# Kernel tuning notes

Hardware: AMD Instinct MI355X
Metric: run time of the kernel (lower is better)

Reference implementation:

```python
import jax, jax.numpy as jnp
import numpy as np

B, L, D, H, NL, F, C = 32, 512, 512, 8, 6, 2048, 9
HD = D // H
SCALE = float(np.sqrt(HD))
EPS = 1e-5


def _layernorm(x, g, b):
    mu = jnp.mean(x, axis=-1, keepdims=True)
    var = jnp.mean((x - mu) ** 2, axis=-1, keepdims=True)
    return (x - mu) * jax.lax.rsqrt(var + EPS) * g + b


def setup_inputs() -> dict:
    key = jax.random.key(0)
    ks = jax.random.split(key, 16)
    s = 0.02
    return {
        "x": jax.random.normal(ks[0], (B, L, D), jnp.float32),
        "case_ids": jax.random.randint(ks[1], (B, L), 0, C),
        "attention_mask": jnp.ones((B, L), jnp.int32),
        "Wq": jax.random.normal(ks[2], (NL, D, D), jnp.float32) * s,
        "bq": jnp.zeros((NL, D), jnp.float32),
        "Wk": jax.random.normal(ks[3], (NL, D, D), jnp.float32) * s,
        "bk": jnp.zeros((NL, D), jnp.float32),
        "Wv": jax.random.normal(ks[4], (NL, D, D), jnp.float32) * s,
        "bv": jnp.zeros((NL, D), jnp.float32),
        "Wo": jax.random.normal(ks[5], (NL, D, D), jnp.float32) * s,
        "bo": jnp.zeros((NL, D), jnp.float32),
        "ln1_g": jnp.ones((NL, D), jnp.float32),
        "ln1_b": jnp.zeros((NL, D), jnp.float32),
        "ln2_g": jnp.ones((NL, D), jnp.float32),
        "ln2_b": jnp.zeros((NL, D), jnp.float32),
        "W1": jax.random.normal(ks[6], (NL, D, F), jnp.float32) * s,
        "b1": jnp.zeros((NL, F), jnp.float32),
        "W2": jax.random.normal(ks[7], (NL, F, D), jnp.float32) * s,
        "b2": jnp.zeros((NL, D), jnp.float32),
        "case_bias": jax.random.normal(ks[8], (NL, H, C, C), jnp.float32) * 0.1,
        "verb_bias": jax.random.normal(ks[9], (NL, H), jnp.float32) * 0.1,
        "fn_g": jnp.ones((D,), jnp.float32),
        "fn_b": jnp.zeros((D,), jnp.float32),
    }


def reference(x, case_ids, attention_mask, Wq, bq, Wk, bk, Wv, bv, Wo, bo,
              ln1_g, ln1_b, ln2_g, ln2_b, W1, b1, W2, b2,
              case_bias, verb_bias, fn_g, fn_b):
    dt = x.dtype
    # causal + padding additive mask: [B, 1, L, L]
    causal = jnp.triu(jnp.full((L, L), -10000.0, dtype=dt), k=1)[None, None]
    pad = (1.0 - attention_mask.astype(dt))[:, None, None, :] * -10000.0
    mask = causal + pad
    verb_mask = (case_ids == 8).astype(dt)  # [B, L]
    ci, cj = case_ids[:, :, None], case_ids[:, None, :]  # [B,L,1], [B,1,L]

    for i in range(NL):
        h = _layernorm(x, ln1_g[i], ln1_b[i])
        q = (h @ Wq[i] + bq[i]).reshape(B, L, H, HD).transpose(0, 2, 1, 3)
        k = (h @ Wk[i] + bk[i]).reshape(B, L, H, HD).transpose(0, 2, 1, 3)
        v = (h @ Wv[i] + bv[i]).reshape(B, L, H, HD).transpose(0, 2, 1, 3)
        scores = jnp.einsum('bhqd,bhkd->bhqk', q, k) / SCALE
        # Panini grammatical bias: per-head pairwise case bias + verb key bias
        pbias = case_bias[i][:, ci, cj]  # [H, B, L, L]
        scores = scores + jnp.transpose(pbias, (1, 0, 2, 3))
        scores = scores + verb_bias[i][None, :, None, None] * verb_mask[:, None, None, :]
        scores = scores + mask
        w = jax.nn.softmax(scores, axis=-1)
        attn = jnp.einsum('bhqk,bhkd->bhqd', w, v).transpose(0, 2, 1, 3).reshape(B, L, D)
        x = x + attn @ Wo[i] + bo[i]
        h2 = _layernorm(x, ln2_g[i], ln2_b[i])
        ff = jax.nn.gelu(h2 @ W1[i] + b1[i], approximate=False) @ W2[i] + b2[i]
        x = x + ff
    return _layernorm(x, fn_g, fn_b)
```

## Files before the change

### kernel.cpp

```cpp
#include <hip/hip_runtime.h>
#include <hip/hip_bf16.h>

#define B_   32
#define L_   512
#define D_   512
#define H_   8
#define NL_  6
#define F_   2048
#define C_   9
#define HD_  64
#define MTOK 16384

typedef __bf16 bf16x8 __attribute__((ext_vector_type(8)));
typedef __bf16 bf16x4 __attribute__((ext_vector_type(4)));
typedef float  f32x4  __attribute__((ext_vector_type(4)));

#define MFMA16(a,b,c) __builtin_amdgcn_mfma_f32_16x16x32_bf16((a),(b),(c),0,0,0)
#define GLD16(g,l) __builtin_amdgcn_global_load_lds( \
    (const __attribute__((address_space(1))) void*)(g), \
    (__attribute__((address_space(3))) void*)(l), 16, 0, 0)

__global__ __launch_bounds__(256) void transpose_w(
    const float* __restrict__ in, __hip_bfloat16* __restrict__ out,
    int K, int N, size_t zso)
{
    __shared__ float t[32][33];
    const int z = blockIdx.z;
    const float* src = in + (size_t)z * K * N;
    __hip_bfloat16* dst = out + (size_t)z * zso;
    const int n0 = blockIdx.x * 32, k0 = blockIdx.y * 32;
    const int tx = threadIdx.x, ty = threadIdx.y;
#pragma unroll
    for (int r = ty; r < 32; r += 8)
        t[r][tx] = src[(size_t)(k0 + r) * N + n0 + tx];
    __syncthreads();
#pragma unroll
    for (int r = ty; r < 32; r += 8)
        dst[(size_t)(n0 + r) * K + k0 + tx] = __float2bfloat16(t[tx][r]);
}

__global__ void copy_f32x4(const float4* __restrict__ in, float4* __restrict__ out, int n)
{
    int i = blockIdx.x * blockDim.x + threadIdx.x;
    if (i < n) out[i] = in[i];
}

template <typename OUT>
__global__ __launch_bounds__(256) void ln_kernel(
    const float* __restrict__ x, const float* __restrict__ g,
    const float* __restrict__ be, OUT* __restrict__ out)
{
    const int row  = blockIdx.x * 4 + (threadIdx.x >> 6);
    const int lane = threadIdx.x & 63;
    const int c0   = lane * 8;
    const float* xr = x + (size_t)row * D_ + c0;
    float4 a = *(const float4*)xr;
    float4 c = *(const float4*)(xr + 4);
    float v[8] = {a.x, a.y, a.z, a.w, c.x, c.y, c.z, c.w};

    float s = 0.f;
#pragma unroll
    for (int j = 0; j < 8; ++j) s += v[j];
#pragma unroll
    for (int o = 1; o < 64; o <<= 1) s += __shfl_xor(s, o, 64);
    const float mu = s * (1.0f / D_);

    float s2 = 0.f;
#pragma unroll
    for (int j = 0; j < 8; ++j) { float d = v[j] - mu; s2 += d * d; }
#pragma unroll
    for (int o = 1; o < 64; o <<= 1) s2 += __shfl_xor(s2, o, 64);
    const float rs = rsqrtf(s2 * (1.0f / D_) + 1e-5f);

    float4 g0 = *(const float4*)(g + c0);
    float4 g1 = *(const float4*)(g + c0 + 4);
    float4 b0 = *(const float4*)(be + c0);
    float4 b1 = *(const float4*)(be + c0 + 4);
    float gg[8] = {g0.x, g0.y, g0.z, g0.w, g1.x, g1.y, g1.z, g1.w};
    float bb[8] = {b0.x, b0.y, b0.z, b0.w, b1.x, b1.y, b1.z, b1.w};

    if constexpr (sizeof(OUT) == 2) {
        bf16x8 o8;
#pragma unroll
        for (int j = 0; j < 8; ++j)
            o8[j] = (__bf16)((v[j] - mu) * rs * gg[j] + bb[j]);
        *(bf16x8*)((__hip_bfloat16*)out + (size_t)row * D_ + c0) = o8;
    } else {
        float* op = (float*)out + (size_t)row * D_ + c0;
        float4 r0, r1;
        r0.x = (v[0]-mu)*rs*gg[0]+bb[0]; r0.y = (v[1]-mu)*rs*gg[1]+bb[1];
        r0.z = (v[2]-mu)*rs*gg[2]+bb[2]; r0.w = (v[3]-mu)*rs*gg[3]+bb[3];
        r1.x = (v[4]-mu)*rs*gg[4]+bb[4]; r1.y = (v[5]-mu)*rs*gg[5]+bb[5];
        r1.z = (v[6]-mu)*rs*gg[6]+bb[6]; r1.w = (v[7]-mu)*rs*gg[7]+bb[7];
        *(float4*)op = r0; *(float4*)(op + 4) = r1;
    }
}

template <int EPI, int WNW>
__global__ __launch_bounds__(512, 2) void gemm_p(
    const __hip_bfloat16* __restrict__ A,
    const __hip_bfloat16* __restrict__ BT,
    const float* __restrict__ bias0, const float* __restrict__ bias1,
    const float* __restrict__ bias2,
    void* __restrict__ out0, void* __restrict__ out1, void* __restrict__ out2,
    const float* __restrict__ Res, int Ndim, int K)
{
    constexpr int FM = (WNW == 4) ? 8 : 4;
    constexpr int BN = WNW * 64;
    constexpr int BLOADS = BN / 128;
    __shared__ __align__(16) __hip_bfloat16 As[4][256 * 32];
    __shared__ __align__(16) __hip_bfloat16 Bs[4][BN * 32];

    const int tid = threadIdx.x;
    const int w = tid >> 6, lane = tid & 63;
    const int lq = lane & 15, lg = lane >> 4;

    const int gX = gridDim.x;
    const int nwg = gX * gridDim.y;
    int flat = blockIdx.y * gX + blockIdx.x;
    {
        const int qq = nwg >> 3, rr = nwg & 7;
        const int xcd = flat & 7, off = flat >> 3;
        flat = (xcd < rr ? xcd * (qq + 1) : rr * (qq + 1) + (xcd - rr) * qq) + off;
    }
    const int bx = flat % gX, by = flat / gX;
    const int m0 = by * 256, n0 = bx * BN;
    const int wm = w / WNW, wn = w % WNW;
    const int RB = wm * (FM * 16);
    const int CB = wn * 64;

    const int sr = lane >> 2;
    const int sc = ((lane & 3) ^ ((lane >> 3) & 3)) * 8;
    const __hip_bfloat16* gA0 = A + (size_t)(m0 + (w*2+0)*16 + sr) * K + sc;
    const __hip_bfloat16* gA1 = A + (size_t)(m0 + (w*2+1)*16 + sr) * K + sc;
    const __hip_bfloat16* gB0;
    const __hip_bfloat16* gB1 = nullptr;
    if constexpr (BLOADS == 2) {
        gB0 = BT + (size_t)(n0 + (w*2+0)*16 + sr) * K + sc;
        gB1 = BT + (size_t)(n0 + (w*2+1)*16 + sr) * K + sc;
    } else {
        gB0 = BT + (size_t)(n0 + w*16 + sr) * K + sc;
    }

    auto STAGE = [&](int tt) {
        const size_t ko = (size_t)tt * 32;
        char* ab = (char*)As[tt & 3];
        GLD16(gA0 + ko, ab + (w*2+0) * 1024);
        GLD16(gA1 + ko, ab + (w*2+1) * 1024);
        char* bb = (char*)Bs[tt & 3];
        if constexpr (BLOADS == 2) {
            GLD16(gB0 + ko, bb + (w*2+0) * 1024);
            GLD16(gB1 + ko, bb + (w*2+1) * 1024);
        } else {
            GLD16(gB0 + ko, bb + w * 1024);
        }
    };

    const int rsw = (lq >> 1) & 3;
    const int aoff = (RB + lq) * 64 + ((lg ^ rsw) << 4);
    const int boff = (CB + lq) * 64 + ((lg ^ rsw) << 4);

    f32x4 acc[FM][4] = {};
    const int NTt = K >> 5;

    STAGE(0); STAGE(1); STAGE(2);

    for (int t = 0; t < NTt; ++t) {
        if (t < NTt - 2) {
            if constexpr (BLOADS == 2) asm volatile("s_waitcnt vmcnt(8)" ::: "memory");
            else                       asm volatile("s_waitcnt vmcnt(6)" ::: "memory");
        } else if (t < NTt - 1) {
            if constexpr (BLOADS == 2) asm volatile("s_waitcnt vmcnt(4)" ::: "memory");
            else                       asm volatile("s_waitcnt vmcnt(3)" ::: "memory");
        } else {
            asm volatile("s_waitcnt vmcnt(0)" ::: "memory");
        }
        __builtin_amdgcn_s_barrier();
        __builtin_amdgcn_sched_barrier(0);

        const char* ca = (const char*)As[t & 3];
        const char* cb = (const char*)Bs[t & 3];
        bf16x8 bf[4];
#pragma unroll
        for (int fn = 0; fn < 4; ++fn) bf[fn] = *(const bf16x8*)(cb + boff + fn * 1024);
        bf16x8 af[FM];
#pragma unroll
        for (int fm = 0; fm < FM; ++fm) af[fm] = *(const bf16x8*)(ca + aoff + fm * 1024);

        if (t + 3 < NTt) STAGE(t + 3);

        __builtin_amdgcn_s_setprio(1);
#pragma unroll
        for (int fm = 0; fm < FM; ++fm)
#pragma unroll
            for (int fn = 0; fn < 4; ++fn)
                acc[fm][fn] = MFMA16(af[fm], bf[fn], acc[fm][fn]);
        __builtin_amdgcn_s_setprio(0);
    }

    if constexpr (EPI == 4) {
        const int sec = n0 >> 9;
        const int nb = (n0 & 511) + CB;
        const float* bp = sec == 0 ? bias0 : (sec == 1 ? bias1 : bias2);
        float bcol[4];
#pragma unroll
        for (int fn = 0; fn < 4; ++fn) bcol[fn] = bp[nb + fn * 16 + lq];
        if (sec < 2) {
            __hip_bfloat16* op = (__hip_bfloat16*)(sec == 0 ? out0 : out1);
#pragma unroll
            for (int fm = 0; fm < FM; ++fm)
#pragma unroll
                for (int fn = 0; fn < 4; ++fn)
#pragma unroll
                    for (int r = 0; r < 4; ++r) {
                        const int m = m0 + RB + fm * 16 + lg * 4 + r;
                        op[(size_t)m * 512 + nb + fn * 16 + lq] =
                            __float2bfloat16(acc[fm][fn][r] + bcol[fn]);
                    }
        } else {
            __hip_bfloat16* vp = (__hip_bfloat16*)out2;
            const int bb = m0 >> 9;
            const int l0 = (m0 & 511) + RB + lg * 4;
#pragma unroll
            for (int fm = 0; fm < FM; ++fm)
#pragma unroll
                for (int fn = 0; fn < 4; ++fn) {
                    bf16x4 pv;
#pragma unroll
                    for (int r = 0; r < 4; ++r)
                        pv[r] = (__bf16)(acc[fm][fn][r] + bcol[fn]);
                    *(bf16x4*)(vp + ((size_t)(bb * 512 + nb + fn * 16 + lq)) * 512
                               + l0 + fm * 16) = pv;
                }
        }
    } else {
        float bcol[4];
#pragma unroll
        for (int fn = 0; fn < 4; ++fn) bcol[fn] = bias0[n0 + CB + fn * 16 + lq];
#pragma unroll
        for (int fm = 0; fm < FM; ++fm)
#pragma unroll
            for (int fn = 0; fn < 4; ++fn) {
                const int n = n0 + CB + fn * 16 + lq;
#pragma unroll
                for (int r = 0; r < 4; ++r) {
                    const int m = m0 + RB + fm * 16 + lg * 4 + r;
                    float v = acc[fm][fn][r] + bcol[fn];
                    if constexpr (EPI == 1) {
                        float* Co = (float*)out0;
                        const size_t idx = (size_t)m * Ndim + n;
                        Co[idx] = Res[idx] + v;
                    } else {
                        float gl = 0.5f * v * (1.0f + erff(v * 0.70710678118654752f));
                        ((__hip_bfloat16*)out0)[(size_t)m * Ndim + n] = __float2bfloat16(gl);
                    }
                }
            }
    }
}

__global__ __launch_bounds__(256) void attn_kernel(
    const __hip_bfloat16* __restrict__ Q, const __hip_bfloat16* __restrict__ K,
    const __hip_bfloat16* __restrict__ VT, __hip_bfloat16* __restrict__ Out,
    const int* __restrict__ case_ids, const int* __restrict__ amask,
    const float* __restrict__ case_bias, const float* __restrict__ verb_bias,
    int layer)
{
    __shared__ __align__(16) __bf16 Ks[2][64 * 64];
    __shared__ __align__(16) __bf16 Vs[2][64 * 64];
    __shared__ __align__(16) __bf16 Pl[4][16 * 64];
    __shared__ __bf16 Bia[9][520];

    const int bh = blockIdx.x;
    const int b = bh >> 3, hh = bh & 7;
    const int qc = blockIdx.y;
    const int t = threadIdx.x;
    const int w = t >> 6, lane = t & 63;
    const int lq = lane & 15, lg = lane >> 4;
    const int swz = lq & 7;

    const int rA = w * 16 + (lane >> 3);
    const int swsrc = ((lane & 7) ^ (lane >> 3)) << 4;
    const __hip_bfloat16* kg0 = K  + ((size_t)b * L_ + rA) * D_ + hh * HD_;
    const __hip_bfloat16* vg0 = VT + ((size_t)b * D_ + hh * HD_ + rA) * L_;

    auto stage = [&](int buf, int kv0) {
        const char* gk = (const char*)(kg0 + (size_t)kv0 * D_) + swsrc;
        GLD16(gk,                      (char*)Ks[buf] + w * 2048);
        GLD16(gk + (size_t)8 * D_ * 2, (char*)Ks[buf] + w * 2048 + 1024);
        const char* gv = (const char*)(vg0 + kv0) + swsrc;
        GLD16(gv,                      (char*)Vs[buf] + w * 2048);
        GLD16(gv + (size_t)8 * L_ * 2, (char*)Vs[buf] + w * 2048 + 1024);
    };

    stage(0, 0);

    const float vb = verb_bias[layer * H_ + hh];
    const float* cb = case_bias + ((size_t)layer * H_ + hh) * (C_ * C_);
    for (int idx = t; idx < 9 * 512; idx += 256) {
        const int ci = idx >> 9, kv = idx & 511;
        const int cj = case_ids[b * L_ + kv];
        Bia[ci][kv] = (__bf16)(cb[ci * C_ + cj] + (cj == 8 ? vb : 0.f)
                               - 10000.f * (1.f - (float)amask[b * L_ + kv]));
    }
    __syncthreads();

    const int qloc = w * 16 + lq;
    const int qrow = qc * 64 + qloc;
    const int ci_q = case_ids[b * L_ + qrow];
    const __hip_bfloat16* qp = Q + ((size_t)b * L_ + qrow) * D_ + hh * HD_;
    const bf16x8 qf0 = *(const bf16x8*)(qp + lg * 8);
    const bf16x8 qf1 = *(const bf16x8*)(qp + 32 + lg * 8);

    float m_run = -1e30f, l_run = 0.f;
    f32x4 o[4] = {};
    const int ntiles = qc + 1;
    int cur = 0;

    for (int kt = 0; kt < ntiles; ++kt) {
        if (kt + 1 < ntiles) stage(cur ^ 1, (kt + 1) * 64);

        const char* kb  = (const char*)Ks[cur];
        const char* vb2 = (const char*)Vs[cur];

        f32x4 s[4] = {};
        __builtin_amdgcn_s_setprio(1);
#pragma unroll
        for (int c = 0; c < 4; ++c) {
            const bf16x8 ka = *(const bf16x8*)(kb + (16 * c + lq) * 128 + ((lg ^ swz) << 4));
            s[c] = MFMA16(ka, qf0, s[c]);
            const bf16x8 kc = *(const bf16x8*)(kb + (16 * c + lq) * 128 + (((4 + lg) ^ swz) << 4));
            s[c] = MFMA16(kc, qf1, s[c]);
        }
        __builtin_amdgcn_s_setprio(0);

        const __bf16* brow = &Bia[ci_q][kt * 64];
        const bool dtile = (kt == qc);
        float xs[16];
#pragma unroll
        for (int c = 0; c < 4; ++c) {
            const bf16x4 bb = *(const bf16x4*)(brow + 16 * c + lg * 4);
#pragma unroll
            for (int r = 0; r < 4; ++r) {
                const int kvl = 16 * c + lg * 4 + r;
                float v = s[c][r] * 0.125f + (float)bb[r];
                xs[4 * c + r] = (dtile && (kvl > qloc)) ? -1e9f : v;
            }
        }

        float a0 = fmaxf(fmaxf(xs[0], xs[1]),  fmaxf(xs[2], xs[3]));
        float a1 = fmaxf(fmaxf(xs[4], xs[5]),  fmaxf(xs[6], xs[7]));
        float a2 = fmaxf(fmaxf(xs[8], xs[9]),  fmaxf(xs[10], xs[11]));
        float a3 = fmaxf(fmaxf(xs[12], xs[13]), fmaxf(xs[14], xs[15]));
        float pmax = fmaxf(fmaxf(a0, a1), fmaxf(a2, a3));
        pmax = fmaxf(pmax, __shfl_xor(pmax, 16, 64));
        pmax = fmaxf(pmax, __shfl_xor(pmax, 32, 64));

        const float mnew = fmaxf(m_run, pmax);
        const float corr = __expf(m_run - mnew);
        float p[16], ps0 = 0.f, ps1 = 0.f;
#pragma unroll
        for (int j = 0; j < 16; j += 2) {
            p[j]     = __expf(xs[j] - mnew);     ps0 += p[j];
            p[j + 1] = __expf(xs[j + 1] - mnew); ps1 += p[j + 1];
        }
        float ps = ps0 + ps1;
        ps += __shfl_xor(ps, 16, 64);
        ps += __shfl_xor(ps, 32, 64);
        l_run = l_run * corr + ps;
        m_run = mnew;

        float cr[4];
#pragma unroll
        for (int r = 0; r < 4; ++r) cr[r] = __shfl(corr, lg * 4 + r, 64);
#pragma unroll
        for (int nt = 0; nt < 4; ++nt)
#pragma unroll
            for (int r = 0; r < 4; ++r) o[nt][r] *= cr[r];

        char* pw = (char*)Pl[w];
#pragma unroll
        for (int c = 0; c < 4; ++c) {
            bf16x4 pv;
#pragma unroll
            for (int r = 0; r < 4; ++r) pv[r] = (__bf16)p[4 * c + r];
            const int slot = (2 * c + (lg >> 1)) ^ swz;
            *(bf16x4*)(pw + lq * 128 + (slot << 4) + ((lg & 1) << 3)) = pv;
        }

        __builtin_amdgcn_s_setprio(1);
#pragma unroll
        for (int hf = 0; hf < 2; ++hf) {
            const bf16x8 pf = *(const bf16x8*)(pw + lq * 128 + (((hf * 4 + lg) ^ swz) << 4));
#pragma unroll
            for (int nt = 0; nt < 4; ++nt) {
                const bf16x8 vf = *(const bf16x8*)(vb2 + (nt * 16 + lq) * 128
                                                   + (((hf * 4 + lg) ^ swz) << 4));
                o[nt] = MFMA16(pf, vf, o[nt]);
            }
        }
        __builtin_amdgcn_s_setprio(0);

        __syncthreads();
        cur ^= 1;
    }

    const float inv = 1.f / l_run;
    float ir[4];
#pragma unroll
    for (int r = 0; r < 4; ++r) ir[r] = __shfl(inv, lg * 4 + r, 64);
    __hip_bfloat16* op = Out + ((size_t)b * L_ + qc * 64 + w * 16) * D_ + hh * HD_;
#pragma unroll
    for (int nt = 0; nt < 4; ++nt)
#pragma unroll
        for (int r = 0; r < 4; ++r)
            op[(size_t)(lg * 4 + r) * D_ + nt * 16 + lq] = __float2bfloat16(o[nt][r] * ir[r]);
}

extern "C" void kernel_launch(void* const* d_in, const int* in_sizes, int n_in,
                              void* d_out, int out_size, void* d_ws, size_t ws_size,
                              hipStream_t stream)
{
    const float* x_in  = (const float*)d_in[0];
    const int*   cids  = (const int*)  d_in[1];
    const int*   amask = (const int*)  d_in[2];
    const float* Wq = (const float*)d_in[3];
    const float* bq = (const float*)d_in[4];
    const float* Wk = (const float*)d_in[5];
    const float* bk = (const float*)d_in[6];
    const float* Wv = (const float*)d_in[7];
    const float* bv = (const float*)d_in[8];
    const float* Wo = (const float*)d_in[9];
    const float* bo = (const float*)d_in[10];
    const float* ln1g = (const float*)d_in[11];
    const float* ln1b = (const float*)d_in[12];
    const float* ln2g = (const float*)d_in[13];
    const float* ln2b = (const float*)d_in[14];
    const float* W1 = (const float*)d_in[15];
    const float* b1 = (const float*)d_in[16];
    const float* W2 = (const float*)d_in[17];
    const float* b2 = (const float*)d_in[18];
    const float* cbias = (const float*)d_in[19];
    const float* vbias = (const float*)d_in[20];
    const float* fng = (const float*)d_in[21];
    const float* fnb = (const float*)d_in[22];

    char* w = (char*)d_ws;
    float* x_ws = (float*)w;                 w += (size_t)MTOK * D_ * 4;
    __hip_bfloat16* hbuf = (__hip_bfloat16*)w; w += (size_t)MTOK * D_ * 2;
    __hip_bfloat16* qbuf = (__hip_bfloat16*)w; w += (size_t)MTOK * D_ * 2;
    __hip_bfloat16* kbuf = (__hip_bfloat16*)w; w += (size_t)MTOK * D_ * 2;
    __hip_bfloat16* vtb  = (__hip_bfloat16*)w; w += (size_t)MTOK * D_ * 2;
    __hip_bfloat16* ffb  = (__hip_bfloat16*)w; w += (size_t)MTOK * F_ * 2;
    __hip_bfloat16* WqkvT = (__hip_bfloat16*)w; w += (size_t)NL_ * 3 * D_ * D_ * 2;
    __hip_bfloat16* WoT  = (__hip_bfloat16*)w; w += (size_t)NL_ * D_ * D_ * 2;
    __hip_bfloat16* W1T  = (__hip_bfloat16*)w; w += (size_t)NL_ * D_ * F_ * 2;
    __hip_bfloat16* W2T  = (__hip_bfloat16*)w; w += (size_t)NL_ * D_ * F_ * 2;

    const size_t qkvZ = (size_t)3 * D_ * D_;
    const dim3 tb(32, 8);
    transpose_w<<<dim3(D_/32, D_/32, NL_), tb, 0, stream>>>(Wq, WqkvT,           D_, D_, qkvZ);
    transpose_w<<<dim3(D_/32, D_/32, NL_), tb, 0, stream>>>(Wk, WqkvT + D_*D_,   D_, D_, qkvZ);
    transpose_w<<<dim3(D_/32, D_/32, NL_), tb, 0, stream>>>(Wv, WqkvT + 2*D_*D_, D_, D_, qkvZ);
    transpose_w<<<dim3(D_/32, D_/32, NL_), tb, 0, stream>>>(Wo, WoT, D_, D_, (size_t)D_*D_);
    transpose_w<<<dim3(F_/32, D_/32, NL_), tb, 0, stream>>>(W1, W1T, D_, F_, (size_t)D_*F_);
    transpose_w<<<dim3(D_/32, F_/32, NL_), tb, 0, stream>>>(W2, W2T, F_, D_, (size_t)D_*F_);

    copy_f32x4<<<8192, 256, 0, stream>>>((const float4*)x_in, (float4*)x_ws,
                                         MTOK * D_ / 4);

    const dim3 gQKV(6, 64);
    const dim3 gO(4, 64);
    const dim3 gW1(8, 64);
    const dim3 gW2(4, 64);

    for (int i = 0; i < NL_; ++i) {
        ln_kernel<__hip_bfloat16><<<MTOK/4, 256, 0, stream>>>(
            x_ws, ln1g + i * D_, ln1b + i * D_, hbuf);

        gemm_p<4, 4><<<gQKV, 512, 0, stream>>>(hbuf, WqkvT + (size_t)i * qkvZ,
            bq + i*D_, bk + i*D_, bv + i*D_, qbuf, kbuf, vtb, nullptr, 512, D_);

        attn_kernel<<<dim3(B_ * H_, L_/64), 256, 0, stream>>>(
            qbuf, kbuf, vtb, hbuf, cids, amask, cbias, vbias, i);

        gemm_p<1, 2><<<gO, 512, 0, stream>>>(hbuf, WoT + (size_t)i*D_*D_,
            bo + i*D_, nullptr, nullptr, x_ws, nullptr, nullptr, x_ws, D_, D_);

        ln_kernel<__hip_bfloat16><<<MTOK/4, 256, 0, stream>>>(
            x_ws, ln2g + i * D_, ln2b + i * D_, hbuf);

        gemm_p<2, 4><<<gW1, 512, 0, stream>>>(hbuf, W1T + (size_t)i*D_*F_,
            b1 + i*F_, nullptr, nullptr, ffb, nullptr, nullptr, nullptr, F_, D_);

        gemm_p<1, 2><<<gW2, 512, 0, stream>>>(ffb, W2T + (size_t)i*D_*F_,
            b2 + i*D_, nullptr, nullptr, x_ws, nullptr, nullptr, x_ws, D_, F_);
    }

    ln_kernel<float><<<MTOK/4, 256, 0, stream>>>(x_ws, fng, fnb, (float*)d_out);
}
```

Baseline: 1.404 ms.

## Shrink GEMM tiles to 4x4 fragments per wave with triple-buffered LDS

```diff
diff --git a/kernel.cpp b/kernel.cpp
--- a/kernel.cpp
+++ b/kernel.cpp
@@ -96,8 +96,8 @@
     }
 }
 
-template <int EPI, int WNW>
-__global__ __launch_bounds__(512, 2) void gemm_p(
+template <int EPI, int WM>
+__global__ __launch_bounds__(WM * 128, (WM == 4) ? 4 : 3) void gemm_r5(
     const __hip_bfloat16* __restrict__ A,
     const __hip_bfloat16* __restrict__ BT,
     const float* __restrict__ bias0, const float* __restrict__ bias1,
@@ -105,15 +105,16 @@
     void* __restrict__ out0, void* __restrict__ out1, void* __restrict__ out2,
     const float* __restrict__ Res, int Ndim, int K)
 {
-    constexpr int FM = (WNW == 4) ? 8 : 4;
-    constexpr int BN = WNW * 64;
-    constexpr int BLOADS = BN / 128;
-    __shared__ __align__(16) __hip_bfloat16 As[4][256 * 32];
-    __shared__ __align__(16) __hip_bfloat16 Bs[4][BN * 32];
+    constexpr int THREADS = WM * 128;
+    constexpr int BM = WM * 64;
+    __shared__ __align__(16) __hip_bfloat16 As[3][BM * 32];
+    __shared__ __align__(16) __hip_bfloat16 Bs[3][128 * 32];
 
     const int tid = threadIdx.x;
     const int w = tid >> 6, lane = tid & 63;
     const int lq = lane & 15, lg = lane >> 4;
+    const int wm = w >> 1, wn = w & 1;
+    const int RB = wm * 64, CB = wn * 64;
 
     const int gX = gridDim.x;
     const int nwg = gX * gridDim.y;
@@ -124,74 +125,57 @@
         flat = (xcd < rr ? xcd * (qq + 1) : rr * (qq + 1) + (xcd - rr) * qq) + off;
     }
     const int bx = flat % gX, by = flat / gX;
-    const int m0 = by * 256, n0 = bx * BN;
-    const int wm = w / WNW, wn = w % WNW;
-    const int RB = wm * (FM * 16);
-    const int CB = wn * 64;
-
-    const int sr = lane >> 2;
-    const int sc = ((lane & 3) ^ ((lane >> 3) & 3)) * 8;
-    const __hip_bfloat16* gA0 = A + (size_t)(m0 + (w*2+0)*16 + sr) * K + sc;
-    const __hip_bfloat16* gA1 = A + (size_t)(m0 + (w*2+1)*16 + sr) * K + sc;
-    const __hip_bfloat16* gB0;
-    const __hip_bfloat16* gB1 = nullptr;
-    if constexpr (BLOADS == 2) {
-        gB0 = BT + (size_t)(n0 + (w*2+0)*16 + sr) * K + sc;
-        gB1 = BT + (size_t)(n0 + (w*2+1)*16 + sr) * K + sc;
-    } else {
-        gB0 = BT + (size_t)(n0 + w*16 + sr) * K + sc;
-    }
+    const int m0 = by * BM, n0 = bx * 128;
+
+    const int rc = tid >> 2;
+    const int sc = ((tid & 3) ^ ((rc >> 1) & 3)) * 8;
+    const __hip_bfloat16* gA0 = A  + (size_t)(m0 + rc) * K + sc;
+    const __hip_bfloat16* gB0 = BT + (size_t)(n0 + rc) * K + sc;
 
     auto STAGE = [&](int tt) {
         const size_t ko = (size_t)tt * 32;
-        char* ab = (char*)As[tt & 3];
-        GLD16(gA0 + ko, ab + (w*2+0) * 1024);
-        GLD16(gA1 + ko, ab + (w*2+1) * 1024);
-        char* bb = (char*)Bs[tt & 3];
-        if constexpr (BLOADS == 2) {
-            GLD16(gB0 + ko, bb + (w*2+0) * 1024);
-            GLD16(gB1 + ko, bb + (w*2+1) * 1024);
-        } else {
-            GLD16(gB0 + ko, bb + w * 1024);
-        }
+        const int sl = tt % 3;
+        char* ab = (char*)As[sl] + w * 1024;
+        GLD16(gA0 + ko, ab);
+        GLD16(gA0 + (size_t)(THREADS / 4) * K + ko, ab + THREADS * 16);
+        char* bb = (char*)Bs[sl] + w * 1024;
+        GLD16(gB0 + ko, bb);
+        if constexpr (WM == 2)
+            GLD16(gB0 + (size_t)64 * K + ko, bb + 4096);
     };
 
     const int rsw = (lq >> 1) & 3;
     const int aoff = (RB + lq) * 64 + ((lg ^ rsw) << 4);
     const int boff = (CB + lq) * 64 + ((lg ^ rsw) << 4);
 
-    f32x4 acc[FM][4] = {};
+    f32x4 acc[4][4] = {};
     const int NTt = K >> 5;
 
-    STAGE(0); STAGE(1); STAGE(2);
+    STAGE(0); STAGE(1);
 
     for (int t = 0; t < NTt; ++t) {
-        if (t < NTt - 2) {
-            if constexpr (BLOADS == 2) asm volatile("s_waitcnt vmcnt(8)" ::: "memory");
-            else                       asm volatile("s_waitcnt vmcnt(6)" ::: "memory");
-        } else if (t < NTt - 1) {
-            if constexpr (BLOADS == 2) asm volatile("s_waitcnt vmcnt(4)" ::: "memory");
-            else                       asm volatile("s_waitcnt vmcnt(3)" ::: "memory");
+        if (t + 1 < NTt) {
+            if constexpr (WM == 4) asm volatile("s_waitcnt vmcnt(3)" ::: "memory");
+            else                   asm volatile("s_waitcnt vmcnt(4)" ::: "memory");
         } else {
             asm volatile("s_waitcnt vmcnt(0)" ::: "memory");
         }
         __builtin_amdgcn_s_barrier();
         __builtin_amdgcn_sched_barrier(0);
 
-        const char* ca = (const char*)As[t & 3];
-        const char* cb = (const char*)Bs[t & 3];
-        bf16x8 bf[4];
+        const char* ca = (const char*)As[t % 3];
+        const char* cb = (const char*)Bs[t % 3];
+        bf16x8 af[4], bf[4];
+#pragma unroll
+        for (int fm = 0; fm < 4; ++fm) af[fm] = *(const bf16x8*)(ca + aoff + fm * 1024);
 #pragma unroll
         for (int fn = 0; fn < 4; ++fn) bf[fn] = *(const bf16x8*)(cb + boff + fn * 1024);
-        bf16x8 af[FM];
-#pragma unroll
-        for (int fm = 0; fm < FM; ++fm) af[fm] = *(const bf16x8*)(ca + aoff + fm * 1024);
-
-        if (t + 3 < NTt) STAGE(t + 3);
+
+        if (t + 2 < NTt) STAGE(t + 2);
 
         __builtin_amdgcn_s_setprio(1);
 #pragma unroll
-        for (int fm = 0; fm < FM; ++fm)
+        for (int fm = 0; fm < 4; ++fm)
 #pragma unroll
             for (int fn = 0; fn < 4; ++fn)
                 acc[fm][fn] = MFMA16(af[fm], bf[fn], acc[fm][fn]);
@@ -208,7 +192,7 @@
         if (sec < 2) {
             __hip_bfloat16* op = (__hip_bfloat16*)(sec == 0 ? out0 : out1);
 #pragma unroll
-            for (int fm = 0; fm < FM; ++fm)
+            for (int fm = 0; fm < 4; ++fm)
 #pragma unroll
                 for (int fn = 0; fn < 4; ++fn)
 #pragma unroll
@@ -222,7 +206,7 @@
             const int bb = m0 >> 9;
             const int l0 = (m0 & 511) + RB + lg * 4;
 #pragma unroll
-            for (int fm = 0; fm < FM; ++fm)
+            for (int fm = 0; fm < 4; ++fm)
 #pragma unroll
                 for (int fn = 0; fn < 4; ++fn) {
                     bf16x4 pv;
@@ -238,7 +222,7 @@
 #pragma unroll
         for (int fn = 0; fn < 4; ++fn) bcol[fn] = bias0[n0 + CB + fn * 16 + lq];
 #pragma unroll
-        for (int fm = 0; fm < FM; ++fm)
+        for (int fm = 0; fm < 4; ++fm)
 #pragma unroll
             for (int fn = 0; fn < 4; ++fn) {
                 const int n = n0 + CB + fn * 16 + lq;
@@ -469,31 +453,31 @@
     copy_f32x4<<<8192, 256, 0, stream>>>((const float4*)x_in, (float4*)x_ws,
                                          MTOK * D_ / 4);
 
-    const dim3 gQKV(6, 64);
-    const dim3 gO(4, 64);
-    const dim3 gW1(8, 64);
-    const dim3 gW2(4, 64);
+    const dim3 gQKV(12, 64);
+    const dim3 gO(4, 128);
+    const dim3 gW1(16, 64);
+    const dim3 gW2(4, 128);
 
     for (int i = 0; i < NL_; ++i) {
         ln_kernel<__hip_bfloat16><<<MTOK/4, 256, 0, stream>>>(
             x_ws, ln1g + i * D_, ln1b + i * D_, hbuf);
 
-        gemm_p<4, 4><<<gQKV, 512, 0, stream>>>(hbuf, WqkvT + (size_t)i * qkvZ,
+        gemm_r5<4, 4><<<gQKV, 512, 0, stream>>>(hbuf, WqkvT + (size_t)i * qkvZ,
             bq + i*D_, bk + i*D_, bv + i*D_, qbuf, kbuf, vtb, nullptr, 512, D_);
 
         attn_kernel<<<dim3(B_ * H_, L_/64), 256, 0, stream>>>(
             qbuf, kbuf, vtb, hbuf, cids, amask, cbias, vbias, i);
 
-        gemm_p<1, 2><<<gO, 512, 0, stream>>>(hbuf, WoT + (size_t)i*D_*D_,
+        gemm_r5<1, 2><<<gO, 256, 0, stream>>>(hbuf, WoT + (size_t)i*D_*D_,
             bo + i*D_, nullptr, nullptr, x_ws, nullptr, nullptr, x_ws, D_, D_);
 
         ln_kernel<__hip_bfloat16><<<MTOK/4, 256, 0, stream>>>(
             x_ws, ln2g + i * D_, ln2b + i * D_, hbuf);
 
-        gemm_p<2, 4><<<gW1, 512, 0, stream>>>(hbuf, W1T + (size_t)i*D_*F_,
+        gemm_r5<2, 4><<<gW1, 512, 0, stream>>>(hbuf, W1T + (size_t)i*D_*F_,
             b1 + i*F_, nullptr, nullptr, ffb, nullptr, nullptr, nullptr, F_, D_);
 
-        gemm_p<1, 2><<<gW2, 512, 0, stream>>>(ffb, W2T + (size_t)i*D_*F_,
+        gemm_r5<1, 2><<<gW2, 256, 0, stream>>>(ffb, W2T + (size_t)i*D_*F_,
             b2 + i*D_, nullptr, nullptr, x_ws, nullptr, nullptr, x_ws, D_, F_);
     }
 
```

Result: faster. 1.335 ms (-4.9%).
